# Optimization experiments

Hardware: AMD Instinct MI355X
Metric: run time of the kernel (lower is better)

The kernel has to match this reference:

```python
import jax, jax.numpy as jnp
import numpy as np

DIM = 64
HEADS = 4
HEAD_DIM = DIM // HEADS
HIDDEN = DIM * 2
B, N = 8, 2048


def _layernorm(x, g, b, eps=1e-5):
    mu = jnp.mean(x, axis=-1, keepdims=True)
    var = jnp.var(x, axis=-1, keepdims=True)
    return (x - mu) * jax.lax.rsqrt(var + eps) * g + b


def setup_inputs() -> dict:
    key = jax.random.key(0)
    ks = jax.random.split(key, 12)
    s = 0.02
    return {
        "x": jax.random.normal(ks[0], (B, N, DIM), jnp.float32),
        "clinic": jax.random.normal(ks[1], (B, N, DIM), jnp.float32),
        "norm1_g": jnp.ones((DIM,), jnp.float32),
        "norm1_b": jnp.zeros((DIM,), jnp.float32),
        "norm2_g": jnp.ones((DIM,), jnp.float32),
        "norm2_b": jnp.zeros((DIM,), jnp.float32),
        "Wkv": jax.random.normal(ks[2], (DIM, 2 * DIM), jnp.float32) * s,
        "bkv": jnp.zeros((2 * DIM,), jnp.float32),
        "Wq": jax.random.normal(ks[3], (DIM, DIM), jnp.float32) * s,
        "bq": jnp.zeros((DIM,), jnp.float32),
        "Wproj": jax.random.normal(ks[4], (DIM, DIM), jnp.float32) * s,
        "bproj": jnp.zeros((DIM,), jnp.float32),
        "W1": jax.random.normal(ks[5], (DIM, HIDDEN), jnp.float32) * s,
        "b1": jnp.zeros((HIDDEN,), jnp.float32),
        "W2": jax.random.normal(ks[6], (HIDDEN, DIM), jnp.float32) * s,
        "b2": jnp.zeros((DIM,), jnp.float32),
    }


def reference(x, clinic, norm1_g, norm1_b, norm2_g, norm2_b,
              Wkv, bkv, Wq, bq, Wproj, bproj, W1, b1, W2, b2):
    # shared norm1 on both streams (as in the torch code)
    xn = _layernorm(x, norm1_g, norm1_b)
    cn = _layernorm(clinic, norm1_g, norm1_b)
    scale = HEAD_DIM ** -0.5
    # K/V from x, Q from clinic
    kv = (xn @ Wkv + bkv).reshape(B, N, 2, HEADS, HEAD_DIM)
    k = kv[:, :, 0].transpose(0, 2, 1, 3)  # [B,H,N,hd]
    v = kv[:, :, 1].transpose(0, 2, 1, 3)
    q = (cn @ Wq + bq).reshape(B, N, HEADS, HEAD_DIM).transpose(0, 2, 1, 3)
    attn = jax.nn.softmax(jnp.einsum('bhqd,bhkd->bhqk', q, k) * scale, axis=-1)
    o = jnp.einsum('bhqk,bhkd->bhqd', attn, v).transpose(0, 2, 1, 3).reshape(B, N, DIM)
    o = o @ Wproj + bproj
    # MLP with residual (dropout/drop_path are inference no-ops)
    h = _layernorm(o, norm2_g, norm2_b)
    h = jax.nn.gelu(h @ W1 + b1, approximate=False) @ W2 + b2
    return o + h
```

## Files before the change

### kernel.cpp

```cpp
#include <hip/hip_runtime.h>
#include <hip/hip_bf16.h>
#include <math.h>

#define B_    8
#define N_    2048
#define DIM_  64
#define H_    4
#define HD_   16
#define HID_  128
#define NROWS (B_ * N_)
#define KVB   64
#define QSCALE (0.25f * 1.4426950408889634f)

typedef float    f32x4 __attribute__((ext_vector_type(4)));
typedef __fp16   hfx2  __attribute__((ext_vector_type(2)));
typedef _Float16 f16x4 __attribute__((ext_vector_type(4)));
typedef _Float16 f16x8 __attribute__((ext_vector_type(8)));

#define MFMA16(a, b, c) __builtin_amdgcn_mfma_f32_16x16x16f16((a), (b), (c), 0, 0, 0)

__device__ __forceinline__ float ex2(float x) {
#if __has_builtin(__builtin_amdgcn_exp2f)
    return __builtin_amdgcn_exp2f(x);
#else
    return exp2f(x);
#endif
}

__global__ __launch_bounds__(256) void k1_ln_qkv(
    const float* __restrict__ x, const float* __restrict__ clinic,
    const float* __restrict__ n1g, const float* __restrict__ n1b,
    const float* __restrict__ Wkv, const float* __restrict__ bkv,
    const float* __restrict__ Wq,  const float* __restrict__ bq,
    _Float16* __restrict__ Kd, _Float16* __restrict__ VTd,
    _Float16* __restrict__ Qd)
{
    __shared__ _Float16 WkvT[128][68];
    __shared__ _Float16 WqT [64][68];
    __shared__ _Float16 xnT [64][68];
    __shared__ _Float16 cnT [64][68];

    const int tid  = threadIdx.x;
    const int row0 = blockIdx.x * 64;

    for (int i = tid; i < 64 * 128; i += 256) {
        const int d = i >> 7, c = i & 127;
        WkvT[c][d] = (_Float16)Wkv[i];
    }
    for (int i = tid; i < 64 * 64; i += 256) {
        const int d = i >> 6, c = i & 63;
        WqT[c][d] = (_Float16)Wq[i];
    }

    {
        const int r = tid >> 4, s = tid & 15;
        const float4 gv = *(const float4*)(n1g + s * 4);
        const float4 bv = *(const float4*)(n1b + s * 4);
        #pragma unroll
        for (int it = 0; it < 4; ++it) {
            const int rl = it * 16 + r;
            const int rg = row0 + rl;
            float4 xv = *(const float4*)(x      + (size_t)rg * DIM_ + s * 4);
            float4 cv = *(const float4*)(clinic + (size_t)rg * DIM_ + s * 4);

            float xs = xv.x + xv.y + xv.z + xv.w;
            float cs = cv.x + cv.y + cv.z + cv.w;
            #pragma unroll
            for (int m = 1; m < 16; m <<= 1) {
                xs += __shfl_xor(xs, m);
                cs += __shfl_xor(cs, m);
            }
            const float xmu = xs * (1.f / 64.f);
            const float cmu = cs * (1.f / 64.f);
            float4 xd = make_float4(xv.x - xmu, xv.y - xmu, xv.z - xmu, xv.w - xmu);
            float4 cd = make_float4(cv.x - cmu, cv.y - cmu, cv.z - cmu, cv.w - cmu);

            float xq = xd.x * xd.x + xd.y * xd.y + xd.z * xd.z + xd.w * xd.w;
            float cq = cd.x * cd.x + cd.y * cd.y + cd.z * cd.z + cd.w * cd.w;
            #pragma unroll
            for (int m = 1; m < 16; m <<= 1) {
                xq += __shfl_xor(xq, m);
                cq += __shfl_xor(cq, m);
            }
            const float xinv = rsqrtf(xq * (1.f / 64.f) + 1e-5f);
            const float cinv = rsqrtf(cq * (1.f / 64.f) + 1e-5f);

            xnT[rl][s * 4 + 0] = (_Float16)(xd.x * xinv * gv.x + bv.x);
            xnT[rl][s * 4 + 1] = (_Float16)(xd.y * xinv * gv.y + bv.y);
            xnT[rl][s * 4 + 2] = (_Float16)(xd.z * xinv * gv.z + bv.z);
            xnT[rl][s * 4 + 3] = (_Float16)(xd.w * xinv * gv.w + bv.w);
            cnT[rl][s * 4 + 0] = (_Float16)(cd.x * cinv * gv.x + bv.x);
            cnT[rl][s * 4 + 1] = (_Float16)(cd.y * cinv * gv.y + bv.y);
            cnT[rl][s * 4 + 2] = (_Float16)(cd.z * cinv * gv.z + bv.z);
            cnT[rl][s * 4 + 3] = (_Float16)(cd.w * cinv * gv.w + bv.w);
        }
    }
    __syncthreads();

    const int lane = tid & 63, wave = tid >> 6;
    const int col  = lane & 15;
    const int grp4 = (lane >> 4) * 4;
    const int arow = wave * 16 + col;
    const f32x4 Z = {0.f, 0.f, 0.f, 0.f};

    f16x4 ax[4], ac[4];
    #pragma unroll
    for (int kt = 0; kt < 4; ++kt) {
        ax[kt] = *(const f16x4*)&xnT[arow][kt * 16 + grp4];
        ac[kt] = *(const f16x4*)&cnT[arow][kt * 16 + grp4];
    }

    const int rg0 = row0 + wave * 16 + grp4;
    const int b   = rg0 >> 11;
    const int n0  = rg0 & (N_ - 1);

    #pragma unroll
    for (int ct = 0; ct < 8; ++ct) {
        f32x4 acc = Z;
        #pragma unroll
        for (int kt = 0; kt < 4; ++kt) {
            const f16x4 bf = *(const f16x4*)&WkvT[ct * 16 + col][kt * 16 + grp4];
            acc = MFMA16(ax[kt], bf, acc);
        }
        const int c = ct * 16 + col;
        const float bias = bkv[c];
        const int hh = (c >> 4) & 3, dd = c & 15;
        if (c & 64) {
            f16x4 v4;
            #pragma unroll
            for (int r = 0; r < 4; ++r) v4[r] = (_Float16)(acc[r] + bias);
            *(f16x4*)(VTd + (((size_t)(b * H_ + hh)) * HD_ + dd) * N_ + n0) = v4;
        } else {
            #pragma unroll
            for (int r = 0; r < 4; ++r)
                Kd[(((size_t)(b * H_ + hh)) * N_ + n0 + r) * HD_ + dd] =
                    (_Float16)(acc[r] + bias);
        }
    }
    #pragma unroll
    for (int ct = 0; ct < 4; ++ct) {
        f32x4 acc = Z;
        #pragma unroll
        for (int kt = 0; kt < 4; ++kt) {
            const f16x4 bf = *(const f16x4*)&WqT[ct * 16 + col][kt * 16 + grp4];
            acc = MFMA16(ac[kt], bf, acc);
        }
        const int c = ct * 16 + col;
        const float bias = bq[c];
        const int hh = c >> 4, dd = c & 15;
        #pragma unroll
        for (int r = 0; r < 4; ++r)
            Qd[(((size_t)(b * H_ + hh)) * N_ + n0 + r) * HD_ + dd] =
                (_Float16)((acc[r] + bias) * QSCALE);
    }
}

__global__ __launch_bounds__(256, 4) void k2_attn(
    const _Float16* __restrict__ Kd, const _Float16* __restrict__ VTd,
    const _Float16* __restrict__ Qd, float* __restrict__ O)
{
    __shared__ float smO[4][64][18];
    __shared__ float smL[4][64];

    const int tid  = threadIdx.x;
    const int lane = tid & 63;
    const int wave = tid >> 6;
    const int col  = lane & 15;
    const int grp4 = (lane >> 4) * 4;

    const int wg = (blockIdx.x & 7) * 128 + (blockIdx.x >> 3);
    const int bh = wg >> 5;
    const int qt = wg & 31;

    const _Float16* Kbh = Kd  + (size_t)bh * (N_ * HD_);
    const _Float16* Vbh = VTd + (size_t)bh * (HD_ * N_);
    const _Float16* Qbh = Qd  + (size_t)bh * (N_ * HD_);

    const int qbase = qt * 64;
    f16x4 qf[4];
    #pragma unroll
    for (int qp = 0; qp < 4; ++qp)
        qf[qp] = *(const f16x4*)(Qbh + (qbase + qp * 16 + col) * HD_ + grp4);

    const int k0   = wave * 512;
    const int koff = (k0 + col) * HD_ + grp4;
    const int voff = col * N_ + k0 + grp4;

    float l0 = 0.f, l1 = 0.f, l2 = 0.f, l3 = 0.f;
    f32x4 o0 = {0.f, 0.f, 0.f, 0.f}, o1 = o0, o2 = o0, o3 = o0;

    f16x4 kf[4], vf[4];
    #pragma unroll
    for (int sb = 0; sb < 4; ++sb) {
        kf[sb] = *(const f16x4*)(Kbh + koff + sb * (16 * HD_));
        vf[sb] = *(const f16x4*)(Vbh + voff + sb * 16);
    }

    for (int kt = 0; kt < 8; ++kt) {
        const int nx = (kt + 1) & 7;
        f16x4 kn[4], vn[4];
        #pragma unroll
        for (int sb = 0; sb < 4; ++sb) {
            kn[sb] = *(const f16x4*)(Kbh + koff + nx * (KVB * HD_) + sb * (16 * HD_));
            vn[sb] = *(const f16x4*)(Vbh + voff + nx * KVB + sb * 16);
        }

        const f32x4 Z = {0.f, 0.f, 0.f, 0.f};
        #pragma unroll
        for (int qp = 0; qp < 4; ++qp) {
            f32x4 s[4];
            #pragma unroll
            for (int sb = 0; sb < 4; ++sb)
                s[sb] = MFMA16(kf[sb], qf[qp], Z);

            float pl = 0.f;
            f16x4 pf[4];
            #pragma unroll
            for (int sb = 0; sb < 4; ++sb) {
                const float a0 = ex2(s[sb][0]), a1 = ex2(s[sb][1]);
                const float a2 = ex2(s[sb][2]), a3 = ex2(s[sb][3]);
                pl += (a0 + a1) + (a2 + a3);
                const hfx2 lo = __builtin_amdgcn_cvt_pkrtz(a0, a1);
                const hfx2 hi = __builtin_amdgcn_cvt_pkrtz(a2, a3);
                pf[sb] = (f16x4){(_Float16)lo[0], (_Float16)lo[1],
                                 (_Float16)hi[0], (_Float16)hi[1]};
            }
            if (qp == 0) { l0 += pl; }
            else if (qp == 1) { l1 += pl; }
            else if (qp == 2) { l2 += pl; }
            else { l3 += pl; }

            f32x4& o = (qp == 0) ? o0 : (qp == 1) ? o1 : (qp == 2) ? o2 : o3;
            #pragma unroll
            for (int sb = 0; sb < 4; ++sb)
                o = MFMA16(pf[sb], vf[sb], o);
        }

        #pragma unroll
        for (int sb = 0; sb < 4; ++sb) { kf[sb] = kn[sb]; vf[sb] = vn[sb]; }
    }

    l0 += __shfl_xor(l0, 16); l0 += __shfl_xor(l0, 32);
    l1 += __shfl_xor(l1, 16); l1 += __shfl_xor(l1, 32);
    l2 += __shfl_xor(l2, 16); l2 += __shfl_xor(l2, 32);
    l3 += __shfl_xor(l3, 16); l3 += __shfl_xor(l3, 32);

    #pragma unroll
    for (int r = 0; r < 4; ++r) {
        smO[wave][ 0 + grp4 + r][col] = o0[r];
        smO[wave][16 + grp4 + r][col] = o1[r];
        smO[wave][32 + grp4 + r][col] = o2[r];
        smO[wave][48 + grp4 + r][col] = o3[r];
    }
    if ((lane >> 4) == 0) {
        smL[wave][ 0 + col] = l0;
        smL[wave][16 + col] = l1;
        smL[wave][32 + col] = l2;
        smL[wave][48 + col] = l3;
    }
    __syncthreads();

    {
        const int q = tid >> 2, h4 = (tid & 3) * 4;
        const float ls = smL[0][q] + smL[1][q] + smL[2][q] + smL[3][q];
        const float rl = 1.f / ls;
        float v[4];
        #pragma unroll
        for (int j = 0; j < 4; ++j)
            v[j] = (smO[0][q][h4 + j] + smO[1][q][h4 + j] +
                    smO[2][q][h4 + j] + smO[3][q][h4 + j]) * rl;
        const int b = bh >> 2, h = bh & 3;
        float* dst = O + ((size_t)b * N_ + qbase + q) * DIM_ + h * HD_ + h4;
        *(float4*)dst = make_float4(v[0], v[1], v[2], v[3]);
    }
}

__device__ __forceinline__ float gelu_fast(float v) {
    const float t = v * v;
    const float z = v * fmaf(0.035677408f, t, 0.79788456f);
    const float e = ex2(z * 2.8853900817779268f);
    const float r = __builtin_amdgcn_rcpf(e + 1.0f);
    return v * e * r;
}

__global__ __launch_bounds__(256) void k3_proj_mlp(
    const float* __restrict__ O,
    const float* __restrict__ Wproj, const float* __restrict__ bproj,
    const float* __restrict__ n2g,   const float* __restrict__ n2b,
    const float* __restrict__ W1,    const float* __restrict__ b1,
    const float* __restrict__ W2,    const float* __restrict__ b2,
    float* __restrict__ out)
{
    __shared__ _Float16 WpT [64][68];
    __shared__ _Float16 W1T [128][68];
    __shared__ _Float16 W2T [64][136];
    __shared__ _Float16 aT  [64][68];
    __shared__ float    sp  [64][68];
    __shared__ _Float16 hT  [64][68];
    __shared__ _Float16 actT[64][136];

    const int tid  = threadIdx.x;
    const int row0 = blockIdx.x * 64;

    for (int i = tid; i < 64 * 64; i += 256) {
        const int k = i >> 6, c = i & 63;
        WpT[c][k] = (_Float16)Wproj[i];
    }
    for (int i = tid; i < 64 * 128; i += 256) {
        const int k = i >> 7, c = i & 127;
        W1T[c][k] = (_Float16)W1[i];
    }
    for (int i = tid; i < 128 * 64; i += 256) {
        const int k = i >> 6, c = i & 63;
        W2T[c][k] = (_Float16)W2[i];
    }
    {
        const int r = tid >> 2, c0 = (tid & 3) * 16;
        const float4* src = (const float4*)(O + (size_t)(row0 + r) * DIM_ + c0);
        #pragma unroll
        for (int j = 0; j < 4; ++j) {
            const float4 v = src[j];
            aT[r][c0 + j * 4 + 0] = (_Float16)v.x;
            aT[r][c0 + j * 4 + 1] = (_Float16)v.y;
            aT[r][c0 + j * 4 + 2] = (_Float16)v.z;
            aT[r][c0 + j * 4 + 3] = (_Float16)v.w;
        }
    }
    __syncthreads();

    const int lane = tid & 63, wave = tid >> 6;
    const int col  = lane & 15;
    const int grp4 = (lane >> 4) * 4;
    const int arow = wave * 16 + col;
    const f32x4 Z = {0.f, 0.f, 0.f, 0.f};

    {
        f16x4 af[4];
        #pragma unroll
        for (int kt = 0; kt < 4; ++kt)
            af[kt] = *(const f16x4*)&aT[arow][kt * 16 + grp4];
        #pragma unroll
        for (int ct = 0; ct < 4; ++ct) {
            f32x4 acc = Z;
            #pragma unroll
            for (int kt = 0; kt < 4; ++kt) {
                const f16x4 bf = *(const f16x4*)&WpT[ct * 16 + col][kt * 16 + grp4];
                acc = MFMA16(af[kt], bf, acc);
            }
            const int c = ct * 16 + col;
            const float bias = bproj[c];
            #pragma unroll
            for (int r = 0; r < 4; ++r)
                sp[wave * 16 + grp4 + r][c] = acc[r] + bias;
        }
    }
    __syncthreads();

    {
        const int r = tid >> 4, s = tid & 15;
        const float4 gv = *(const float4*)(n2g + s * 4);
        const float4 bv = *(const float4*)(n2b + s * 4);
        #pragma unroll
        for (int it = 0; it < 4; ++it) {
            const int rl = it * 16 + r;
            const float4 v = *(const float4*)&sp[rl][s * 4];
            float sm = v.x + v.y + v.z + v.w;
            #pragma unroll
            for (int m = 1; m < 16; m <<= 1) sm += __shfl_xor(sm, m);
            const float mu = sm * (1.f / 64.f);
            float4 d4 = make_float4(v.x - mu, v.y - mu, v.z - mu, v.w - mu);
            float qs = d4.x * d4.x + d4.y * d4.y + d4.z * d4.z + d4.w * d4.w;
            #pragma unroll
            for (int m = 1; m < 16; m <<= 1) qs += __shfl_xor(qs, m);
            const float inv = rsqrtf(qs * (1.f / 64.f) + 1e-5f);
            hT[rl][s * 4 + 0] = (_Float16)(d4.x * inv * gv.x + bv.x);
            hT[rl][s * 4 + 1] = (_Float16)(d4.y * inv * gv.y + bv.y);
            hT[rl][s * 4 + 2] = (_Float16)(d4.z * inv * gv.z + bv.z);
            hT[rl][s * 4 + 3] = (_Float16)(d4.w * inv * gv.w + bv.w);
        }
    }
    __syncthreads();

    {
        f16x4 hf[4];
        #pragma unroll
        for (int kt = 0; kt < 4; ++kt)
            hf[kt] = *(const f16x4*)&hT[arow][kt * 16 + grp4];
        #pragma unroll
        for (int ct = 0; ct < 8; ++ct) {
            f32x4 acc = Z;
            #pragma unroll
            for (int kt = 0; kt < 4; ++kt) {
                const f16x4 bf = *(const f16x4*)&W1T[ct * 16 + col][kt * 16 + grp4];
                acc = MFMA16(hf[kt], bf, acc);
            }
            const int c = ct * 16 + col;
            const float bias = b1[c];
            #pragma unroll
            for (int r = 0; r < 4; ++r)
                actT[wave * 16 + grp4 + r][c] =
                    (_Float16)gelu_fast(acc[r] + bias);
        }
    }

    {
        f16x4 pf[8];
        #pragma unroll
        for (int kt = 0; kt < 8; ++kt)
            pf[kt] = *(const f16x4*)&actT[arow][kt * 16 + grp4];
        #pragma unroll
        for (int ct = 0; ct < 4; ++ct) {
            f32x4 acc = Z;
            #pragma unroll
            for (int kt = 0; kt < 8; ++kt) {
                const f16x4 bf = *(const f16x4*)&W2T[ct * 16 + col][kt * 16 + grp4];
                acc = MFMA16(pf[kt], bf, acc);
            }
            const int c = ct * 16 + col;
            const float bias = b2[c];
            #pragma unroll
            for (int r = 0; r < 4; ++r) {
                const int rl = wave * 16 + grp4 + r;
                out[(size_t)(row0 + rl) * DIM_ + c] = acc[r] + bias + sp[rl][c];
            }
        }
    }
}

extern "C" void kernel_launch(void* const* d_in, const int* in_sizes, int n_in,
                              void* d_out, int out_size, void* d_ws, size_t ws_size,
                              hipStream_t stream) {
    const float* x      = (const float*)d_in[0];
    const float* clinic = (const float*)d_in[1];
    const float* n1g    = (const float*)d_in[2];
    const float* n1b    = (const float*)d_in[3];
    const float* n2g    = (const float*)d_in[4];
    const float* n2b    = (const float*)d_in[5];
    const float* Wkv    = (const float*)d_in[6];
    const float* bkv    = (const float*)d_in[7];
    const float* Wq     = (const float*)d_in[8];
    const float* bq     = (const float*)d_in[9];
    const float* Wproj  = (const float*)d_in[10];
    const float* bproj  = (const float*)d_in[11];
    const float* W1     = (const float*)d_in[12];
    const float* b1     = (const float*)d_in[13];
    const float* W2     = (const float*)d_in[14];
    const float* b2     = (const float*)d_in[15];
    float* out = (float*)d_out;

    char* ws = (char*)d_ws;
    const size_t SZ = (size_t)B_ * H_ * N_ * HD_;
    _Float16* Kd  = (_Float16*)ws;
    _Float16* VTd = (_Float16*)(ws + 2 * SZ);
    _Float16* Qd  = (_Float16*)(ws + 4 * SZ);
    float*    O   = (float*)   (ws + 6 * SZ);

    k1_ln_qkv<<<NROWS / 64, 256, 0, stream>>>(x, clinic, n1g, n1b, Wkv, bkv,
                                              Wq, bq, Kd, VTd, Qd);
    k2_attn<<<32 * 32, 256, 0, stream>>>(Kd, VTd, Qd, O);
    k3_proj_mlp<<<NROWS / 64, 256, 0, stream>>>(O, Wproj, bproj, n2g, n2b,
                                                W1, b1, W2, b2, out);
}
```

Baseline: 44.18 us.

## Double block size in LN/QKV and MLP kernels, vectorize loads, alias shared buffers

```diff
diff --git a/kernel.cpp b/kernel.cpp
--- a/kernel.cpp
+++ b/kernel.cpp
@@ -27,7 +27,7 @@
 #endif
 }
 
-__global__ __launch_bounds__(256) void k1_ln_qkv(
+__global__ __launch_bounds__(512) void k1_ln_qkv(
     const float* __restrict__ x, const float* __restrict__ clinic,
     const float* __restrict__ n1g, const float* __restrict__ n1b,
     const float* __restrict__ Wkv, const float* __restrict__ bkv,
@@ -43,13 +43,23 @@
     const int tid  = threadIdx.x;
     const int row0 = blockIdx.x * 64;
 
-    for (int i = tid; i < 64 * 128; i += 256) {
-        const int d = i >> 7, c = i & 127;
-        WkvT[c][d] = (_Float16)Wkv[i];
-    }
-    for (int i = tid; i < 64 * 64; i += 256) {
-        const int d = i >> 6, c = i & 63;
-        WqT[c][d] = (_Float16)Wq[i];
+    #pragma unroll
+    for (int i = tid; i < 2048; i += 512) {
+        const float4 w = ((const float4*)Wkv)[i];
+        const int e = i * 4, d = e >> 7, c = e & 127;
+        WkvT[c + 0][d] = (_Float16)w.x;
+        WkvT[c + 1][d] = (_Float16)w.y;
+        WkvT[c + 2][d] = (_Float16)w.z;
+        WkvT[c + 3][d] = (_Float16)w.w;
+    }
+    #pragma unroll
+    for (int i = tid; i < 1024; i += 512) {
+        const float4 w = ((const float4*)Wq)[i];
+        const int e = i * 4, d = e >> 6, c = e & 63;
+        WqT[c + 0][d] = (_Float16)w.x;
+        WqT[c + 1][d] = (_Float16)w.y;
+        WqT[c + 2][d] = (_Float16)w.z;
+        WqT[c + 3][d] = (_Float16)w.w;
     }
 
     {
@@ -57,8 +67,8 @@
         const float4 gv = *(const float4*)(n1g + s * 4);
         const float4 bv = *(const float4*)(n1b + s * 4);
         #pragma unroll
-        for (int it = 0; it < 4; ++it) {
-            const int rl = it * 16 + r;
+        for (int it = 0; it < 2; ++it) {
+            const int rl = it * 32 + r;
             const int rg = row0 + rl;
             float4 xv = *(const float4*)(x      + (size_t)rg * DIM_ + s * 4);
             float4 cv = *(const float4*)(clinic + (size_t)rg * DIM_ + s * 4);
@@ -85,14 +95,17 @@
             const float xinv = rsqrtf(xq * (1.f / 64.f) + 1e-5f);
             const float cinv = rsqrtf(cq * (1.f / 64.f) + 1e-5f);
 
-            xnT[rl][s * 4 + 0] = (_Float16)(xd.x * xinv * gv.x + bv.x);
-            xnT[rl][s * 4 + 1] = (_Float16)(xd.y * xinv * gv.y + bv.y);
-            xnT[rl][s * 4 + 2] = (_Float16)(xd.z * xinv * gv.z + bv.z);
-            xnT[rl][s * 4 + 3] = (_Float16)(xd.w * xinv * gv.w + bv.w);
-            cnT[rl][s * 4 + 0] = (_Float16)(cd.x * cinv * gv.x + bv.x);
-            cnT[rl][s * 4 + 1] = (_Float16)(cd.y * cinv * gv.y + bv.y);
-            cnT[rl][s * 4 + 2] = (_Float16)(cd.z * cinv * gv.z + bv.z);
-            cnT[rl][s * 4 + 3] = (_Float16)(cd.w * cinv * gv.w + bv.w);
+            f16x4 xo, co;
+            xo[0] = (_Float16)(xd.x * xinv * gv.x + bv.x);
+            xo[1] = (_Float16)(xd.y * xinv * gv.y + bv.y);
+            xo[2] = (_Float16)(xd.z * xinv * gv.z + bv.z);
+            xo[3] = (_Float16)(xd.w * xinv * gv.w + bv.w);
+            co[0] = (_Float16)(cd.x * cinv * gv.x + bv.x);
+            co[1] = (_Float16)(cd.y * cinv * gv.y + bv.y);
+            co[2] = (_Float16)(cd.z * cinv * gv.z + bv.z);
+            co[3] = (_Float16)(cd.w * cinv * gv.w + bv.w);
+            *(f16x4*)&xnT[rl][s * 4] = xo;
+            *(f16x4*)&cnT[rl][s * 4] = co;
         }
     }
     __syncthreads();
@@ -100,7 +113,9 @@
     const int lane = tid & 63, wave = tid >> 6;
     const int col  = lane & 15;
     const int grp4 = (lane >> 4) * 4;
-    const int arow = wave * 16 + col;
+    const int rt   = wave & 3;
+    const int half = wave >> 2;
+    const int arow = rt * 16 + col;
     const f32x4 Z = {0.f, 0.f, 0.f, 0.f};
 
     f16x4 ax[4], ac[4];
@@ -110,12 +125,13 @@
         ac[kt] = *(const f16x4*)&cnT[arow][kt * 16 + grp4];
     }
 
-    const int rg0 = row0 + wave * 16 + grp4;
+    const int rg0 = row0 + rt * 16 + grp4;
     const int b   = rg0 >> 11;
     const int n0  = rg0 & (N_ - 1);
 
     #pragma unroll
-    for (int ct = 0; ct < 8; ++ct) {
+    for (int cti = 0; cti < 4; ++cti) {
+        const int ct = half * 4 + cti;
         f32x4 acc = Z;
         #pragma unroll
         for (int kt = 0; kt < 4; ++kt) {
@@ -138,7 +154,8 @@
         }
     }
     #pragma unroll
-    for (int ct = 0; ct < 4; ++ct) {
+    for (int cti = 0; cti < 2; ++cti) {
+        const int ct = half * 2 + cti;
         f32x4 acc = Z;
         #pragma unroll
         for (int kt = 0; kt < 4; ++kt) {
@@ -283,7 +300,7 @@
     return v * e * r;
 }
 
-__global__ __launch_bounds__(256) void k3_proj_mlp(
+__global__ __launch_bounds__(512) void k3_proj_mlp(
     const float* __restrict__ O,
     const float* __restrict__ Wproj, const float* __restrict__ bproj,
     const float* __restrict__ n2g,   const float* __restrict__ n2b,
@@ -291,67 +308,83 @@
     const float* __restrict__ W2,    const float* __restrict__ b2,
     float* __restrict__ out)
 {
-    __shared__ _Float16 WpT [64][68];
-    __shared__ _Float16 W1T [128][68];
-    __shared__ _Float16 W2T [64][136];
-    __shared__ _Float16 aT  [64][68];
-    __shared__ float    sp  [64][68];
-    __shared__ _Float16 hT  [64][68];
-    __shared__ _Float16 actT[64][136];
+    union U1 { _Float16 wp[64][68];  _Float16 h[64][68]; };
+    union U2 { _Float16 a[64][68];   _Float16 act[64][136]; };
+    union U3 { _Float16 w1[128][68]; float outs[64][68]; };
+    __shared__ U1 u1;
+    __shared__ U2 u2;
+    __shared__ U3 u3;
+    __shared__ _Float16 W2T[64][136];
+    __shared__ float    sp [64][68];
 
     const int tid  = threadIdx.x;
     const int row0 = blockIdx.x * 64;
 
-    for (int i = tid; i < 64 * 64; i += 256) {
-        const int k = i >> 6, c = i & 63;
-        WpT[c][k] = (_Float16)Wproj[i];
-    }
-    for (int i = tid; i < 64 * 128; i += 256) {
-        const int k = i >> 7, c = i & 127;
-        W1T[c][k] = (_Float16)W1[i];
-    }
-    for (int i = tid; i < 128 * 64; i += 256) {
-        const int k = i >> 6, c = i & 63;
-        W2T[c][k] = (_Float16)W2[i];
-    }
-    {
-        const int r = tid >> 2, c0 = (tid & 3) * 16;
-        const float4* src = (const float4*)(O + (size_t)(row0 + r) * DIM_ + c0);
-        #pragma unroll
-        for (int j = 0; j < 4; ++j) {
-            const float4 v = src[j];
-            aT[r][c0 + j * 4 + 0] = (_Float16)v.x;
-            aT[r][c0 + j * 4 + 1] = (_Float16)v.y;
-            aT[r][c0 + j * 4 + 2] = (_Float16)v.z;
-            aT[r][c0 + j * 4 + 3] = (_Float16)v.w;
-        }
+    #pragma unroll
+    for (int i = tid; i < 1024; i += 512) {
+        const float4 w = ((const float4*)Wproj)[i];
+        const int e = i * 4, d = e >> 6, c = e & 63;
+        u1.wp[c + 0][d] = (_Float16)w.x;
+        u1.wp[c + 1][d] = (_Float16)w.y;
+        u1.wp[c + 2][d] = (_Float16)w.z;
+        u1.wp[c + 3][d] = (_Float16)w.w;
+    }
+    #pragma unroll
+    for (int i = tid; i < 2048; i += 512) {
+        const float4 w = ((const float4*)W1)[i];
+        const int e = i * 4, d = e >> 7, c = e & 127;
+        u3.w1[c + 0][d] = (_Float16)w.x;
+        u3.w1[c + 1][d] = (_Float16)w.y;
+        u3.w1[c + 2][d] = (_Float16)w.z;
+        u3.w1[c + 3][d] = (_Float16)w.w;
+    }
+    #pragma unroll
+    for (int i = tid; i < 2048; i += 512) {
+        const float4 w = ((const float4*)W2)[i];
+        const int e = i * 4, d = e >> 6, c = e & 63;
+        W2T[c + 0][d] = (_Float16)w.x;
+        W2T[c + 1][d] = (_Float16)w.y;
+        W2T[c + 2][d] = (_Float16)w.z;
+        W2T[c + 3][d] = (_Float16)w.w;
+    }
+    #pragma unroll
+    for (int i = tid; i < 1024; i += 512) {
+        const float4 v = ((const float4*)(O + (size_t)row0 * DIM_))[i];
+        const int e = i * 4, r = e >> 6, c = e & 63;
+        f16x4 h4;
+        h4[0] = (_Float16)v.x; h4[1] = (_Float16)v.y;
+        h4[2] = (_Float16)v.z; h4[3] = (_Float16)v.w;
+        *(f16x4*)&u2.a[r][c] = h4;
     }
     __syncthreads();
 
     const int lane = tid & 63, wave = tid >> 6;
     const int col  = lane & 15;
     const int grp4 = (lane >> 4) * 4;
-    const int arow = wave * 16 + col;
+    const int rt   = wave & 3;
+    const int half = wave >> 2;
+    const int arow = rt * 16 + col;
     const f32x4 Z = {0.f, 0.f, 0.f, 0.f};
 
     {
         f16x4 af[4];
         #pragma unroll
         for (int kt = 0; kt < 4; ++kt)
-            af[kt] = *(const f16x4*)&aT[arow][kt * 16 + grp4];
-        #pragma unroll
-        for (int ct = 0; ct < 4; ++ct) {
+            af[kt] = *(const f16x4*)&u2.a[arow][kt * 16 + grp4];
+        #pragma unroll
+        for (int cti = 0; cti < 2; ++cti) {
+            const int ct = half * 2 + cti;
             f32x4 acc = Z;
             #pragma unroll
             for (int kt = 0; kt < 4; ++kt) {
-                const f16x4 bf = *(const f16x4*)&WpT[ct * 16 + col][kt * 16 + grp4];
+                const f16x4 bf = *(const f16x4*)&u1.wp[ct * 16 + col][kt * 16 + grp4];
                 acc = MFMA16(af[kt], bf, acc);
             }
             const int c = ct * 16 + col;
             const float bias = bproj[c];
             #pragma unroll
             for (int r = 0; r < 4; ++r)
-                sp[wave * 16 + grp4 + r][c] = acc[r] + bias;
+                sp[rt * 16 + grp4 + r][c] = acc[r] + bias;
         }
     }
     __syncthreads();
@@ -361,8 +394,8 @@
         const float4 gv = *(const float4*)(n2g + s * 4);
         const float4 bv = *(const float4*)(n2b + s * 4);
         #pragma unroll
-        for (int it = 0; it < 4; ++it) {
-            const int rl = it * 16 + r;
+        for (int it = 0; it < 2; ++it) {
+            const int rl = it * 32 + r;
             const float4 v = *(const float4*)&sp[rl][s * 4];
             float sm = v.x + v.y + v.z + v.w;
             #pragma unroll
@@ -373,10 +406,12 @@
             #pragma unroll
             for (int m = 1; m < 16; m <<= 1) qs += __shfl_xor(qs, m);
             const float inv = rsqrtf(qs * (1.f / 64.f) + 1e-5f);
-            hT[rl][s * 4 + 0] = (_Float16)(d4.x * inv * gv.x + bv.x);
-            hT[rl][s * 4 + 1] = (_Float16)(d4.y * inv * gv.y + bv.y);
-            hT[rl][s * 4 + 2] = (_Float16)(d4.z * inv * gv.z + bv.z);
-            hT[rl][s * 4 + 3] = (_Float16)(d4.w * inv * gv.w + bv.w);
+            f16x4 ho;
+            ho[0] = (_Float16)(d4.x * inv * gv.x + bv.x);
+            ho[1] = (_Float16)(d4.y * inv * gv.y + bv.y);
+            ho[2] = (_Float16)(d4.z * inv * gv.z + bv.z);
+            ho[3] = (_Float16)(d4.w * inv * gv.w + bv.w);
+            *(f16x4*)&u1.h[rl][s * 4] = ho;
         }
     }
     __syncthreads();
@@ -385,31 +420,34 @@
         f16x4 hf[4];
         #pragma unroll
         for (int kt = 0; kt < 4; ++kt)
-            hf[kt] = *(const f16x4*)&hT[arow][kt * 16 + grp4];
-        #pragma unroll
-        for (int ct = 0; ct < 8; ++ct) {
+            hf[kt] = *(const f16x4*)&u1.h[arow][kt * 16 + grp4];
+        #pragma unroll
+        for (int cti = 0; cti < 4; ++cti) {
+            const int ct = half * 4 + cti;
             f32x4 acc = Z;
             #pragma unroll
             for (int kt = 0; kt < 4; ++kt) {
-                const f16x4 bf = *(const f16x4*)&W1T[ct * 16 + col][kt * 16 + grp4];
+                const f16x4 bf = *(const f16x4*)&u3.w1[ct * 16 + col][kt * 16 + grp4];
                 acc = MFMA16(hf[kt], bf, acc);
             }
             const int c = ct * 16 + col;
             const float bias = b1[c];
             #pragma unroll
             for (int r = 0; r < 4; ++r)
-                actT[wave * 16 + grp4 + r][c] =
+                u2.act[rt * 16 + grp4 + r][c] =
                     (_Float16)gelu_fast(acc[r] + bias);
         }
     }
+    __syncthreads();
 
     {
         f16x4 pf[8];
         #pragma unroll
         for (int kt = 0; kt < 8; ++kt)
-            pf[kt] = *(const f16x4*)&actT[arow][kt * 16 + grp4];
-        #pragma unroll
-        for (int ct = 0; ct < 4; ++ct) {
+            pf[kt] = *(const f16x4*)&u2.act[arow][kt * 16 + grp4];
+        #pragma unroll
+        for (int cti = 0; cti < 2; ++cti) {
+            const int ct = half * 2 + cti;
             f32x4 acc = Z;
             #pragma unroll
             for (int kt = 0; kt < 8; ++kt) {
@@ -419,11 +457,23 @@
             const int c = ct * 16 + col;
             const float bias = b2[c];
             #pragma unroll
-            for (int r = 0; r < 4; ++r) {
-                const int rl = wave * 16 + grp4 + r;
-                out[(size_t)(row0 + rl) * DIM_ + c] = acc[r] + bias + sp[rl][c];
-            }
-        }
+            for (int r = 0; r < 4; ++r)
+                u3.outs[rt * 16 + grp4 + r][c] = acc[r] + bias;
+        }
+    }
+    __syncthreads();
+
+    {
+        const int r = tid >> 3, cg = (tid & 7) * 8;
+        const float4 a0 = *(const float4*)&u3.outs[r][cg];
+        const float4 a1 = *(const float4*)&u3.outs[r][cg + 4];
+        const float4 s0 = *(const float4*)&sp[r][cg];
+        const float4 s1 = *(const float4*)&sp[r][cg + 4];
+        float* op = out + (size_t)(row0 + r) * DIM_ + cg;
+        *(float4*)(op)     = make_float4(a0.x + s0.x, a0.y + s0.y,
+                                         a0.z + s0.z, a0.w + s0.w);
+        *(float4*)(op + 4) = make_float4(a1.x + s1.x, a1.y + s1.y,
+                                         a1.z + s1.z, a1.w + s1.w);
     }
 }
 
@@ -455,9 +505,9 @@
     _Float16* Qd  = (_Float16*)(ws + 4 * SZ);
     float*    O   = (float*)   (ws + 6 * SZ);
 
-    k1_ln_qkv<<<NROWS / 64, 256, 0, stream>>>(x, clinic, n1g, n1b, Wkv, bkv,
+    k1_ln_qkv<<<NROWS / 64, 512, 0, stream>>>(x, clinic, n1g, n1b, Wkv, bkv,
                                               Wq, bq, Kd, VTd, Qd);
     k2_attn<<<32 * 32, 256, 0, stream>>>(Kd, VTd, Qd, O);
-    k3_proj_mlp<<<NROWS / 64, 256, 0, stream>>>(O, Wproj, bproj, n2g, n2b,
+    k3_proj_mlp<<<NROWS / 64, 512, 0, stream>>>(O, Wproj, bproj, n2g, n2b,
                                                 W1, b1, W2, b2, out);
 }
```

Result: no change. 43.79 us (-0.9%).
